# Optimization experiments

Hardware: AMD Instinct MI355X
Metric: run time of the kernel (lower is better)

The kernel has to match this reference:

```python
import jax, jax.numpy as jnp
import numpy as np
import math

B = 8
LATENT = 1024
K_DIM = 128   # conv input channels / view dim k
M_DIM = 256   # attention feature dim m
N = 4096      # points_num // num_branch; attention seq len
EPS = 1e-5


def _bn(h, g, b, m, v):
    # inference-mode BatchNorm1d over [B, C, L]
    return (h - m[None, :, None]) * (g / jnp.sqrt(v + EPS))[None, :, None] + b[None, :, None]


def _conv(h, w, b):
    # Conv1d with kernel_size=1 == channel matmul: h [B,C,L], w [O,C]
    return jnp.einsum('bcl,oc->bol', h, w) + b[None, :, None]


def setup_inputs() -> dict:
    key = jax.random.key(0)
    ks = jax.random.split(key, 64)
    it = iter(range(64))

    def nrm(shape, scale=0.05):
        return jax.random.normal(ks[next(it)], shape, jnp.float32) * scale

    def pos(shape):
        return jax.random.uniform(ks[next(it)], shape, jnp.float32, 0.5, 1.5)

    d = {}
    d['x'] = jax.random.normal(ks[next(it)], (B, LATENT), jnp.float32)
    d['fc1_w'] = nrm((M_DIM * K_DIM, LATENT))
    d['fc1_b'] = nrm((M_DIM * K_DIM,))
    d['c1q_w'] = nrm((64, K_DIM)); d['c1q_b'] = nrm((64,))
    d['c2q_w'] = nrm((128, 64));   d['c2q_b'] = nrm((128,))
    d['c3q_w'] = nrm((N, 128));    d['c3q_b'] = nrm((N,))
    d['c3k_w'] = nrm((N, 128));    d['c3k_b'] = nrm((N,))
    d['c1v_w'] = nrm((64, K_DIM)); d['c1v_b'] = nrm((64,))
    d['c2v_w'] = nrm((128, 64));   d['c2v_b'] = nrm((128,))
    d['c3v_w'] = nrm((N, 128));    d['c3v_b'] = nrm((N,))
    for nm, c in [('bn1q', 64), ('bn2q', 128), ('bn1k', 64), ('bn2k', 128), ('bn1v', 64), ('bn2v', 128)]:
        d[nm + '_g'] = pos((c,))
        d[nm + '_be'] = nrm((c,))
        d[nm + '_m'] = nrm((c,))
        d[nm + '_v'] = pos((c,))
    d['co_w'] = nrm((3, M_DIM)); d['co_b'] = nrm((3,))
    return d


def _forward(x, fc1_w, fc1_b, c1q_w, c1q_b, c2q_w, c2q_b, c3q_w, c3q_b, c3k_w, c3k_b,
             c1v_w, c1v_b, c2v_w, c2v_b, c3v_w, c3v_b,
             bn1q_g, bn1q_be, bn1q_m, bn1q_v, bn2q_g, bn2q_be, bn2q_m, bn2q_v,
             bn1k_g, bn1k_be, bn1k_m, bn1k_v, bn2k_g, bn2k_be, bn2k_m, bn2k_v,
             bn1v_g, bn1v_be, bn1v_m, bn1v_v, bn2v_g, bn2v_be, bn2v_m, bn2v_v,
             co_w, co_b):
    h = (x @ fc1_w.T + fc1_b).reshape(-1, M_DIM, K_DIM)   # [B, m, k]
    h = jnp.transpose(h, (0, 2, 1))                        # [B, k, m]
    # Q path
    Q = jax.nn.relu(_bn(_conv(h, c1q_w, c1q_b), bn1q_g, bn1q_be, bn1q_m, bn1q_v))
    Q = jax.nn.relu(_bn(_conv(Q, c2q_w, c2q_b), bn2q_g, bn2q_be, bn2q_m, bn2q_v))
    Q = _conv(Q, c3q_w, c3q_b)                             # [B, n, m]
    # K path: source re-uses conv1_q / conv2_q weights (faithful to original)
    K = jax.nn.relu(_bn(_conv(h, c1q_w, c1q_b), bn1k_g, bn1k_be, bn1k_m, bn1k_v))
    K = jax.nn.relu(_bn(_conv(K, c2q_w, c2q_b), bn2k_g, bn2k_be, bn2k_m, bn2k_v))
    K = _conv(K, c3k_w, c3k_b)                             # [B, n, m]
    # V path
    V = jax.nn.relu(_bn(_conv(h, c1v_w, c1v_b), bn1v_g, bn1v_be, bn1v_m, bn1v_v))
    V = jax.nn.relu(_bn(_conv(V, c2v_w, c2v_b), bn2v_g, bn2v_be, bn2v_m, bn2v_v))
    V = _conv(V, c3v_w, c3v_b)                             # [B, n, m]
    # hand-rolled attention: scores [B, n, n] (source scales by sqrt(k))
    scores = jnp.einsum('bim,bjm->bij', Q, K) / math.sqrt(K_DIM)
    attn = jax.nn.softmax(scores, axis=2)
    out = jnp.einsum('bij,bjm->bim', attn, V)              # [B, n, m]
    out = jnp.einsum('bnm,om->bon', out, co_w) + co_b[None, :, None]  # [B, 3, n]
    return jnp.transpose(out, (0, 2, 1))                   # [B, n, 3]


def reference(x, fc1_w, fc1_b, c1q_w, c1q_b, c2q_w, c2q_b, c3q_w, c3q_b, c3k_w, c3k_b,
              c1v_w, c1v_b, c2v_w, c2v_b, c3v_w, c3v_b,
              bn1q_g, bn1q_be, bn1q_m, bn1q_v, bn2q_g, bn2q_be, bn2q_m, bn2q_v,
              bn1k_g, bn1k_be, bn1k_m, bn1k_v, bn2k_g, bn2k_be, bn2k_m, bn2k_v,
              bn1v_g, bn1v_be, bn1v_m, bn1v_v, bn2v_g, bn2v_be, bn2v_m, bn2v_v,
              co_w, co_b):
    return _forward(x, fc1_w, fc1_b, c1q_w, c1q_b, c2q_w, c2q_b, c3q_w, c3q_b, c3k_w, c3k_b,
                    c1v_w, c1v_b, c2v_w, c2v_b, c3v_w, c3v_b,
                    bn1q_g, bn1q_be, bn1q_m, bn1q_v, bn2q_g, bn2q_be, bn2q_m, bn2q_v,
                    bn1k_g, bn1k_be, bn1k_m, bn1k_v, bn2k_g, bn2k_be, bn2k_m, bn2k_v,
                    bn1v_g, bn1v_be, bn1v_m, bn1v_v, bn2v_g, bn2v_be, bn2v_m, bn2v_v,
                    co_w, co_b)
```

## Files before the change

kernel.cpp:

```cpp
#include <hip/hip_runtime.h>
#include <cstdint>
#include <cstddef>

#define EPS 1e-5f

typedef __attribute__((ext_vector_type(8))) short bf16x8;
typedef __attribute__((ext_vector_type(4))) float f32x4;
typedef __attribute__((ext_vector_type(16))) float f32x16;

__device__ __forceinline__ unsigned short rne_bf16(float f) {
  union { float f; unsigned int u; } v; v.f = f;
  unsigned int u = v.u;
  return (unsigned short)((u + 0x7fffu + ((u >> 16) & 1u)) >> 16);
}
__device__ __forceinline__ float bf16_to_f(unsigned short h) {
  union { unsigned int u; float f; } v; v.u = ((unsigned int)h) << 16; return v.f;
}
__device__ __forceinline__ void split_hl(float v, unsigned short& h, unsigned short& l) {
  h = rne_bf16(v);
  l = rne_bf16(v - bf16_to_f(h));
}
__device__ __forceinline__ f32x4 mfma16(bf16x8 a, bf16x8 b, f32x4 c) {
  return __builtin_amdgcn_mfma_f32_16x16x32_bf16(a, b, c, 0, 0, 0);
}
__device__ __forceinline__ f32x16 mfma32(bf16x8 a, bf16x8 b, f32x16 c) {
  return __builtin_amdgcn_mfma_f32_32x32x16_bf16(a, b, c, 0, 0, 0);
}

__global__ __launch_bounds__(256) void k_fc1(const float* __restrict__ x,
                                             const float* __restrict__ w,
                                             const float* __restrict__ bias,
                                             float* __restrict__ h_t) {
  const int lane = threadIdx.x & 63;
  const int wv = threadIdx.x >> 6;
  const int r = blockIdx.x * 4 + wv;
  const float4* wr = (const float4*)(w + (size_t)r * 1024);
  float acc[8] = {0, 0, 0, 0, 0, 0, 0, 0};
#pragma unroll
  for (int i = 0; i < 4; ++i) {
    float4 wv4 = wr[lane + i * 64];
#pragma unroll
    for (int b = 0; b < 8; ++b) {
      float4 xv = ((const float4*)(x + b * 1024))[lane + i * 64];
      acc[b] += wv4.x * xv.x + wv4.y * xv.y + wv4.z * xv.z + wv4.w * xv.w;
    }
  }
#pragma unroll
  for (int d = 1; d < 64; d <<= 1) {
#pragma unroll
    for (int b = 0; b < 8; ++b) acc[b] += __shfl_xor(acc[b], d);
  }
  if (lane == 0) {
    const int mm = r >> 7, kk = r & 127;
    const float bb = bias[r];
#pragma unroll
    for (int b = 0; b < 8; ++b) h_t[b * 32768 + kk * 256 + mm] = acc[b] + bb;
  }
}

__global__ __launch_bounds__(256) void k_conv1(
    const float* __restrict__ h_t,
    const float* __restrict__ c1q_w, const float* __restrict__ c1q_b,
    const float* __restrict__ c1v_w, const float* __restrict__ c1v_b,
    const float* __restrict__ g1q, const float* __restrict__ be1q,
    const float* __restrict__ mu1q, const float* __restrict__ va1q,
    const float* __restrict__ g1k, const float* __restrict__ be1k,
    const float* __restrict__ mu1k, const float* __restrict__ va1k,
    const float* __restrict__ g1v, const float* __restrict__ be1v,
    const float* __restrict__ mu1v, const float* __restrict__ va1v,
    float* __restrict__ T1q, float* __restrict__ T1k, float* __restrict__ T1v) {
  const int m = threadIdx.x;
  const int o = blockIdx.x & 63;
  const int b = blockIdx.x >> 6;
  const int path = blockIdx.y;
  const float* w = (path == 0 ? c1q_w : c1v_w) + o * 128;
  const float* h = h_t + b * 32768 + m;
  float acc = 0.f;
#pragma unroll 8
  for (int c = 0; c < 128; ++c) acc += w[c] * h[c * 256];
  if (path == 0) {
    const float z = acc + c1q_b[o];
    const float sq = g1q[o] / sqrtf(va1q[o] + EPS);
    T1q[b * 16384 + o * 256 + m] = fmaxf((z - mu1q[o]) * sq + be1q[o], 0.f);
    const float sk = g1k[o] / sqrtf(va1k[o] + EPS);
    T1k[b * 16384 + o * 256 + m] = fmaxf((z - mu1k[o]) * sk + be1k[o], 0.f);
  } else {
    const float z = acc + c1v_b[o];
    const float sv = g1v[o] / sqrtf(va1v[o] + EPS);
    T1v[b * 16384 + o * 256 + m] = fmaxf((z - mu1v[o]) * sv + be1v[o], 0.f);
  }
}

__global__ __launch_bounds__(256) void k_conv2(
    const float* __restrict__ T1q, const float* __restrict__ T1k,
    const float* __restrict__ T1v,
    const float* __restrict__ c2q_w, const float* __restrict__ c2q_b,
    const float* __restrict__ c2v_w, const float* __restrict__ c2v_b,
    const float* __restrict__ g2q, const float* __restrict__ be2q,
    const float* __restrict__ mu2q, const float* __restrict__ va2q,
    const float* __restrict__ g2k, const float* __restrict__ be2k,
    const float* __restrict__ mu2k, const float* __restrict__ va2k,
    const float* __restrict__ g2v, const float* __restrict__ be2v,
    const float* __restrict__ mu2v, const float* __restrict__ va2v,
    unsigned short* __restrict__ Q2H, unsigned short* __restrict__ Q2L,
    unsigned short* __restrict__ K2H, unsigned short* __restrict__ K2L,
    float* __restrict__ V2F) {
  const int m = threadIdx.x;
  const int b = blockIdx.x;
  const int path = blockIdx.y;
  const int oc = blockIdx.z;
  const float* T1 = (path == 0 ? T1q : path == 1 ? T1k : T1v) + b * 16384 + m;
  const float* w = (path == 2 ? c2v_w : c2q_w);
  const float* cb = (path == 2 ? c2v_b : c2q_b);
  const float* g = (path == 0 ? g2q : path == 1 ? g2k : g2v);
  const float* be = (path == 0 ? be2q : path == 1 ? be2k : be2v);
  const float* mu = (path == 0 ? mu2q : path == 1 ? mu2k : mu2v);
  const float* va = (path == 0 ? va2q : path == 1 ? va2k : va2v);
  float t[64];
#pragma unroll
  for (int c = 0; c < 64; ++c) t[c] = T1[c * 256];
  unsigned short* oh =
      (path == 0 ? Q2H : K2H) + b * 32768 + m * 128 + oc * 64;
  unsigned short* ol =
      (path == 0 ? Q2L : K2L) + b * 32768 + m * 128 + oc * 64;
  for (int og = 0; og < 8; ++og) {
    bf16x8 ph, pl;
#pragma unroll
    for (int j = 0; j < 8; ++j) {
      const int o = oc * 64 + og * 8 + j;
      float acc = cb[o];
      const float* wo = w + o * 64;
#pragma unroll
      for (int c = 0; c < 64; ++c) acc += wo[c] * t[c];
      const float s = g[o] / sqrtf(va[o] + EPS);
      const float val = fmaxf((acc - mu[o]) * s + be[o], 0.f);
      if (path == 2) {
        V2F[b * 32768 + o * 256 + m] = val;
      } else {
        unsigned short hh, ll;
        split_hl(val, hh, ll);
        ph[j] = (short)hh; pl[j] = (short)ll;
      }
    }
    if (path != 2) {
      *(bf16x8*)(oh + og * 8) = ph;
      *(bf16x8*)(ol + og * 8) = pl;
    }
  }
}

__global__ __launch_bounds__(256) void k_conv3all(
    const float* __restrict__ c3q_w, const float* __restrict__ c3q_b,
    const float* __restrict__ c3k_w, const float* __restrict__ c3k_b,
    const unsigned short* __restrict__ Q2H, const unsigned short* __restrict__ Q2L,
    const unsigned short* __restrict__ K2H, const unsigned short* __restrict__ K2L,
    unsigned short* __restrict__ QhB, unsigned short* __restrict__ QlB,
    unsigned short* __restrict__ KhB, unsigned short* __restrict__ KlB,
    const float* __restrict__ c3v_w, const float* __restrict__ c3v_b,
    const float* __restrict__ V2F, const float* __restrict__ co_w,
    float4* __restrict__ Vpp) {
  const int z = blockIdx.z;
  const int b = blockIdx.y;
  if (z == 2) {
    if (blockIdx.x >= 16) return;
    __shared__ float Us[387];
    __shared__ float Up[256][3];
    const int tt = threadIdx.x;
    {
      const int c = tt >> 1, mh = tt & 1;
      const float* v = V2F + b * 32768 + c * 256 + mh * 128;
      const float* cw0 = co_w + mh * 128;
      float u0 = 0.f, u1 = 0.f, u2 = 0.f;
#pragma unroll 4
      for (int mm = 0; mm < 128; ++mm) {
        const float xv = v[mm];
        u0 += xv * cw0[mm];
        u1 += xv * cw0[256 + mm];
        u2 += xv * cw0[512 + mm];
      }
      Up[tt][0] = u0; Up[tt][1] = u1; Up[tt][2] = u2;
      if (tt < 3) {
        float s = 0.f;
        for (int mm = 0; mm < 256; ++mm) s += co_w[tt * 256 + mm];
        Us[384 + tt] = s;
      }
    }
    __syncthreads();
    if ((tt & 1) == 0) {
      const int c = tt >> 1;
      Us[c * 3 + 0] = Up[tt][0] + Up[tt + 1][0];
      Us[c * 3 + 1] = Up[tt][1] + Up[tt + 1][1];
      Us[c * 3 + 2] = Up[tt][2] + Up[tt + 1][2];
    }
    __syncthreads();
    const int n = blockIdx.x * 256 + tt;
    const float* w = c3v_w + (size_t)n * 128;
    float a0 = 0.f, a1 = 0.f, a2 = 0.f;
#pragma unroll 4
    for (int c = 0; c < 128; ++c) {
      const float wc = w[c];
      a0 += wc * Us[c * 3 + 0];
      a1 += wc * Us[c * 3 + 1];
      a2 += wc * Us[c * 3 + 2];
    }
    const float bb = c3v_b[n];
    Vpp[(size_t)b * 4096 + n] =
        make_float4(a0 + bb * Us[384], a1 + bb * Us[385], a2 + bb * Us[386], 0.f);
    return;
  }
  const float* W = (z == 0) ? c3q_w : c3k_w;
  const float* bias = (z == 0) ? c3q_b : c3k_b;
  const unsigned short* Xh = (z == 0) ? Q2H : K2H;
  const unsigned short* Xl = (z == 0) ? Q2L : K2L;
  unsigned short* Yh = (z == 0) ? QhB : KhB;
  unsigned short* Yl = (z == 0) ? QlB : KlB;
  const float scale = (z == 0) ? 0.08838834764831845f * 1.4426950408889634f : 1.0f;
  const int lane = threadIdx.x & 63, wv = threadIdx.x >> 6;
  const int l15 = lane & 15, quad = lane >> 4;
  const unsigned short* XH = Xh + b * 32768;
  const unsigned short* XL = Xl + b * 32768;
  unsigned short* YH = Yh + (size_t)b * 4096 * 256;
  unsigned short* YL = Yl + (size_t)b * 4096 * 256;
  const int nb = blockIdx.x * 64 + wv * 16;
  const float* wr = W + (size_t)(nb + l15) * 128 + quad * 8;
  bf16x8 ah[4], al[4];
#pragma unroll
  for (int ks = 0; ks < 4; ++ks) {
#pragma unroll
    for (int j = 0; j < 8; ++j) {
      unsigned short hh, ll;
      split_hl(wr[ks * 32 + j], hh, ll);
      ah[ks][j] = (short)hh; al[ks][j] = (short)ll;
    }
  }
  f32x4 acc[16];
#pragma unroll
  for (int ms = 0; ms < 16; ++ms) acc[ms] = (f32x4){0, 0, 0, 0};
#pragma unroll
  for (int ks = 0; ks < 4; ++ks) {
#pragma unroll
    for (int ms = 0; ms < 16; ++ms) {
      const size_t off = (size_t)(ms * 16 + l15) * 128 + ks * 32 + quad * 8;
      bf16x8 bh = *(const bf16x8*)(XH + off);
      bf16x8 bl = *(const bf16x8*)(XL + off);
      acc[ms] = mfma16(ah[ks], bh, acc[ms]);
      acc[ms] = mfma16(al[ks], bh, acc[ms]);
      acc[ms] = mfma16(ah[ks], bl, acc[ms]);
    }
  }
#pragma unroll
  for (int r = 0; r < 4; ++r) {
    const int n = nb + quad * 4 + r;
    const float bv = bias[n];
#pragma unroll
    for (int ms = 0; ms < 16; ++ms) {
      const float v = (acc[ms][r] + bv) * scale;
      unsigned short hh, ll;
      split_hl(v, hh, ll);
      YH[(size_t)n * 256 + ms * 16 + l15] = hh;
      YL[(size_t)n * 256 + ms * 16 + l15] = ll;
    }
  }
}

__global__ __launch_bounds__(256, 2) void k_attn(
    const unsigned short* __restrict__ Qh, const unsigned short* __restrict__ Ql,
    const unsigned short* __restrict__ Kh, const unsigned short* __restrict__ Kl,
    const float4* __restrict__ Vpp, float4* __restrict__ part) {
  __shared__ __align__(16) short Kt[2][2][32 * 264];
  __shared__ __align__(16) float4 Vt[2][32];
  const int t = threadIdx.x;
  const int lane = t & 63, wv = t >> 6;
  const int l31 = lane & 31, half = lane >> 5;
  const int b = blockIdx.x & 7;
  const int qt = (blockIdx.x >> 3) & 31;
  const int jh = blockIdx.x >> 8;
  const int qrow = qt * 128 + wv * 32 + l31;
  const size_t qoff = ((size_t)b * 4096 + qrow) * 256 + half * 8;
  bf16x8 qfh[16], qfl[16];
#pragma unroll
  for (int kc = 0; kc < 16; ++kc) {
    qfh[kc] = *(const bf16x8*)(Qh + qoff + kc * 16);
    qfl[kc] = *(const bf16x8*)(Ql + qoff + kc * 16);
  }
  const unsigned short* Kgh = Kh + (size_t)b * 4096 * 256;
  const unsigned short* Kgl = Kl + (size_t)b * 4096 * 256;
  const float4* Vg = Vpp + (size_t)b * 4096;
  const int r0 = t >> 5;
  const int sseg = (t & 31) * 8;
  float a0 = 0.f, a1 = 0.f, a2 = 0.f, al = 0.f;
  const int jt0 = jh * 64;
  {
    const int jbase = jt0 * 32;
#pragma unroll
    for (int i = 0; i < 4; ++i) {
      const int row = i * 8 + r0;
      const size_t g = (size_t)(jbase + row) * 256 + sseg;
      *(bf16x8*)&Kt[0][0][row * 264 + sseg] = *(const bf16x8*)(Kgh + g);
      *(bf16x8*)&Kt[0][1][row * 264 + sseg] = *(const bf16x8*)(Kgl + g);
    }
    if (t < 32) Vt[0][t] = Vg[jbase + t];
  }
  __syncthreads();
  for (int it = 0; it < 64; ++it) {
    const int cur = it & 1, nxt = cur ^ 1;
    const bool pf = (it < 63);
    bf16x8 th[4], tl[4];
    float4 vpf = make_float4(0.f, 0.f, 0.f, 0.f);
    if (pf) {
      const int jb2 = (jt0 + it + 1) * 32;
#pragma unroll
      for (int i = 0; i < 4; ++i) {
        const size_t g = (size_t)(jb2 + i * 8 + r0) * 256 + sseg;
        th[i] = *(const bf16x8*)(Kgh + g);
        tl[i] = *(const bf16x8*)(Kgl + g);
      }
      if (t < 32) vpf = Vg[jb2 + t];
    }
    f32x16 sA, sB;
#pragma unroll
    for (int r = 0; r < 16; ++r) { sA[r] = 0.f; sB[r] = 0.f; }
    const short* KH = Kt[cur][0];
    const short* KL = Kt[cur][1];
#pragma unroll
    for (int kc = 0; kc < 16; ++kc) {
      bf16x8 kh = *(const bf16x8*)&KH[l31 * 264 + kc * 16 + half * 8];
      bf16x8 kl = *(const bf16x8*)&KL[l31 * 264 + kc * 16 + half * 8];
      sA = mfma32(kh, qfh[kc], sA);
      sB = mfma32(kh, qfl[kc], sB);
      sA = mfma32(kl, qfh[kc], sA);
    }
#pragma unroll
    for (int r = 0; r < 16; ++r) {
      const float p = __builtin_amdgcn_exp2f(sA[r] + sB[r]);
      const float4 vj = Vt[cur][(r & 3) + 8 * (r >> 2) + 4 * half];
      a0 += p * vj.x; a1 += p * vj.y; a2 += p * vj.z; al += p;
    }
    if (pf) {
#pragma unroll
      for (int i = 0; i < 4; ++i) {
        const int row = i * 8 + r0;
        *(bf16x8*)&Kt[nxt][0][row * 264 + sseg] = th[i];
        *(bf16x8*)&Kt[nxt][1][row * 264 + sseg] = tl[i];
      }
      if (t < 32) Vt[nxt][t] = vpf;
    }
    __syncthreads();
  }
  a0 += __shfl_xor(a0, 32);
  a1 += __shfl_xor(a1, 32);
  a2 += __shfl_xor(a2, 32);
  al += __shfl_xor(al, 32);
  if (half == 0)
    part[(size_t)jh * 32768 + (size_t)b * 4096 + qrow] =
        make_float4(a0, a1, a2, al);
}

__global__ __launch_bounds__(256) void k_combine(
    const float4* __restrict__ part, const float* __restrict__ co_b,
    float* __restrict__ out) {
  const int i = blockIdx.x * 256 + threadIdx.x;
  const float4 pa = part[i];
  const float4 pb = part[32768 + i];
  const float rl = 1.f / (pa.w + pb.w);
  const float b0 = co_b[0], b1 = co_b[1], b2 = co_b[2];
  out[(size_t)i * 3 + 0] = (pa.x + pb.x) * rl + b0;
  out[(size_t)i * 3 + 1] = (pa.y + pb.y) * rl + b1;
  out[(size_t)i * 3 + 2] = (pa.z + pb.z) * rl + b2;
}

extern "C" void kernel_launch(void* const* d_in, const int* in_sizes, int n_in,
                              void* d_out, int out_size, void* d_ws, size_t ws_size,
                              hipStream_t stream) {
  const float* x = (const float*)d_in[0];
  const float* fc1_w = (const float*)d_in[1];
  const float* fc1_b = (const float*)d_in[2];
  const float* c1q_w = (const float*)d_in[3];
  const float* c1q_b = (const float*)d_in[4];
  const float* c2q_w = (const float*)d_in[5];
  const float* c2q_b = (const float*)d_in[6];
  const float* c3q_w = (const float*)d_in[7];
  const float* c3q_b = (const float*)d_in[8];
  const float* c3k_w = (const float*)d_in[9];
  const float* c3k_b = (const float*)d_in[10];
  const float* c1v_w = (const float*)d_in[11];
  const float* c1v_b = (const float*)d_in[12];
  const float* c2v_w = (const float*)d_in[13];
  const float* c2v_b = (const float*)d_in[14];
  const float* c3v_w = (const float*)d_in[15];
  const float* c3v_b = (const float*)d_in[16];
  const float* bn1q_g = (const float*)d_in[17];
  const float* bn1q_be = (const float*)d_in[18];
  const float* bn1q_m = (const float*)d_in[19];
  const float* bn1q_v = (const float*)d_in[20];
  const float* bn2q_g = (const float*)d_in[21];
  const float* bn2q_be = (const float*)d_in[22];
  const float* bn2q_m = (const float*)d_in[23];
  const float* bn2q_v = (const float*)d_in[24];
  const float* bn1k_g = (const float*)d_in[25];
  const float* bn1k_be = (const float*)d_in[26];
  const float* bn1k_m = (const float*)d_in[27];
  const float* bn1k_v = (const float*)d_in[28];
  const float* bn2k_g = (const float*)d_in[29];
  const float* bn2k_be = (const float*)d_in[30];
  const float* bn2k_m = (const float*)d_in[31];
  const float* bn2k_v = (const float*)d_in[32];
  const float* bn1v_g = (const float*)d_in[33];
  const float* bn1v_be = (const float*)d_in[34];
  const float* bn1v_m = (const float*)d_in[35];
  const float* bn1v_v = (const float*)d_in[36];
  const float* bn2v_g = (const float*)d_in[37];
  const float* bn2v_be = (const float*)d_in[38];
  const float* bn2v_m = (const float*)d_in[39];
  const float* bn2v_v = (const float*)d_in[40];
  const float* co_w = (const float*)d_in[41];
  const float* co_b = (const float*)d_in[42];

  char* ws = (char*)d_ws;
  float* h_t = (float*)(ws + 0);
  float* T1q = (float*)(ws + 1048576);
  float* T1k = (float*)(ws + 1572864);
  float* T1v = (float*)(ws + 2097152);
  unsigned short* Q2H = (unsigned short*)(ws + 2621440);
  unsigned short* Q2L = (unsigned short*)(ws + 3145728);
  unsigned short* K2H = (unsigned short*)(ws + 3670016);
  unsigned short* K2L = (unsigned short*)(ws + 4194304);
  float* V2F = (float*)(ws + 4718592);
  unsigned short* QhB = (unsigned short*)(ws + 5767168);
  unsigned short* QlB = (unsigned short*)(ws + 22544384);
  unsigned short* KhB = (unsigned short*)(ws + 39321600);
  unsigned short* KlB = (unsigned short*)(ws + 56098816);
  float4* Vpp = (float4*)(ws + 72876032);
  float4* part = (float4*)(ws + 73416704);

  k_fc1<<<8192, 256, 0, stream>>>(x, fc1_w, fc1_b, h_t);
  k_conv1<<<dim3(512, 2), 256, 0, stream>>>(
      h_t, c1q_w, c1q_b, c1v_w, c1v_b,
      bn1q_g, bn1q_be, bn1q_m, bn1q_v,
      bn1k_g, bn1k_be, bn1k_m, bn1k_v,
      bn1v_g, bn1v_be, bn1v_m, bn1v_v,
      T1q, T1k, T1v);
  k_conv2<<<dim3(8, 3, 2), 256, 0, stream>>>(
      T1q, T1k, T1v, c2q_w, c2q_b, c2v_w, c2v_b,
      bn2q_g, bn2q_be, bn2q_m, bn2q_v,
      bn2k_g, bn2k_be, bn2k_m, bn2k_v,
      bn2v_g, bn2v_be, bn2v_m, bn2v_v,
      Q2H, Q2L, K2H, K2L, V2F);
  k_conv3all<<<dim3(64, 8, 3), 256, 0, stream>>>(
      c3q_w, c3q_b, c3k_w, c3k_b, Q2H, Q2L, K2H, K2L,
      QhB, QlB, KhB, KlB, c3v_w, c3v_b, V2F, co_w, Vpp);
  k_attn<<<512, 256, 0, stream>>>(QhB, QlB, KhB, KlB, Vpp, part);
  k_combine<<<128, 256, 0, stream>>>(part, co_b, (float*)d_out);
}
```

Measured before the change: 666.8 us.

## Fuse split-K combine into attention via atomics and add independent MFMA accumulator

Removes the separate combine kernel. Each of the two key-range blocks now atomically adds its partial numerator and denominator into a zeroed buffer, and the second block to finish, found through an atomic counter, normalises and writes the output. A third accumulator breaks the dependent MFMA chain on sA, and s_setprio raises wave priority around the MFMA loop. In exchange it adds a memset launch, atomic traffic and an extra register tile, which may pressure occupancy.

```diff
diff --git a/kernel.cpp b/kernel.cpp
--- a/kernel.cpp
+++ b/kernel.cpp
@@ -266,7 +266,9 @@
 __global__ __launch_bounds__(256, 2) void k_attn(
     const unsigned short* __restrict__ Qh, const unsigned short* __restrict__ Ql,
     const unsigned short* __restrict__ Kh, const unsigned short* __restrict__ Kl,
-    const float4* __restrict__ Vpp, float4* __restrict__ part) {
+    const float4* __restrict__ Vpp, float* __restrict__ partsum,
+    unsigned int* __restrict__ cnt, const float* __restrict__ co_b,
+    float* __restrict__ out) {
   __shared__ __align__(16) short Kt[2][2][32 * 264];
   __shared__ __align__(16) float4 Vt[2][32];
   const int t = threadIdx.x;
@@ -317,22 +319,24 @@
       }
       if (t < 32) vpf = Vg[jb2 + t];
     }
-    f32x16 sA, sB;
-#pragma unroll
-    for (int r = 0; r < 16; ++r) { sA[r] = 0.f; sB[r] = 0.f; }
+    f32x16 sA, sB, sC;
+#pragma unroll
+    for (int r = 0; r < 16; ++r) { sA[r] = 0.f; sB[r] = 0.f; sC[r] = 0.f; }
     const short* KH = Kt[cur][0];
     const short* KL = Kt[cur][1];
+    __builtin_amdgcn_s_setprio(1);
 #pragma unroll
     for (int kc = 0; kc < 16; ++kc) {
       bf16x8 kh = *(const bf16x8*)&KH[l31 * 264 + kc * 16 + half * 8];
       bf16x8 kl = *(const bf16x8*)&KL[l31 * 264 + kc * 16 + half * 8];
       sA = mfma32(kh, qfh[kc], sA);
       sB = mfma32(kh, qfl[kc], sB);
-      sA = mfma32(kl, qfh[kc], sA);
-    }
+      sC = mfma32(kl, qfh[kc], sC);
+    }
+    __builtin_amdgcn_s_setprio(0);
 #pragma unroll
     for (int r = 0; r < 16; ++r) {
-      const float p = __builtin_amdgcn_exp2f(sA[r] + sB[r]);
+      const float p = __builtin_amdgcn_exp2f(sA[r] + sB[r] + sC[r]);
       const float4 vj = Vt[cur][(r & 3) + 8 * (r >> 2) + 4 * half];
       a0 += p * vj.x; a1 += p * vj.y; a2 += p * vj.z; al += p;
     }
@@ -351,22 +355,26 @@
   a1 += __shfl_xor(a1, 32);
   a2 += __shfl_xor(a2, 32);
   al += __shfl_xor(al, 32);
-  if (half == 0)
-    part[(size_t)jh * 32768 + (size_t)b * 4096 + qrow] =
-        make_float4(a0, a1, a2, al);
-}
-
-__global__ __launch_bounds__(256) void k_combine(
-    const float4* __restrict__ part, const float* __restrict__ co_b,
-    float* __restrict__ out) {
-  const int i = blockIdx.x * 256 + threadIdx.x;
-  const float4 pa = part[i];
-  const float4 pb = part[32768 + i];
-  const float rl = 1.f / (pa.w + pb.w);
-  const float b0 = co_b[0], b1 = co_b[1], b2 = co_b[2];
-  out[(size_t)i * 3 + 0] = (pa.x + pb.x) * rl + b0;
-  out[(size_t)i * 3 + 1] = (pa.y + pb.y) * rl + b1;
-  out[(size_t)i * 3 + 2] = (pa.z + pb.z) * rl + b2;
+  if (half == 0) {
+    const int idx = b * 4096 + qrow;
+    float* ps = partsum + (size_t)idx * 4;
+    atomicAdd(ps + 0, a0);
+    atomicAdd(ps + 1, a1);
+    atomicAdd(ps + 2, a2);
+    atomicAdd(ps + 3, al);
+    __threadfence();
+    const unsigned int old = atomicAdd(&cnt[idx], 1u);
+    if (old == 1u) {
+      const float s0 = atomicAdd(ps + 0, 0.f);
+      const float s1 = atomicAdd(ps + 1, 0.f);
+      const float s2 = atomicAdd(ps + 2, 0.f);
+      const float sl = atomicAdd(ps + 3, 0.f);
+      const float rl = 1.f / sl;
+      out[(size_t)idx * 3 + 0] = s0 * rl + co_b[0];
+      out[(size_t)idx * 3 + 1] = s1 * rl + co_b[1];
+      out[(size_t)idx * 3 + 2] = s2 * rl + co_b[2];
+    }
+  }
 }
 
 extern "C" void kernel_launch(void* const* d_in, const int* in_sizes, int n_in,
@@ -431,7 +439,10 @@
   unsigned short* KhB = (unsigned short*)(ws + 39321600);
   unsigned short* KlB = (unsigned short*)(ws + 56098816);
   float4* Vpp = (float4*)(ws + 72876032);
-  float4* part = (float4*)(ws + 73416704);
+  float* partsum = (float*)(ws + 73416704);
+  unsigned int* cnt = (unsigned int*)(ws + 73940992);
+
+  hipMemsetAsync(ws + 73416704, 0, 524288 + 131072, stream);
 
   k_fc1<<<8192, 256, 0, stream>>>(x, fc1_w, fc1_b, h_t);
   k_conv1<<<dim3(512, 2), 256, 0, stream>>>(
@@ -449,6 +460,6 @@
   k_conv3all<<<dim3(64, 8, 3), 256, 0, stream>>>(
       c3q_w, c3q_b, c3k_w, c3k_b, Q2H, Q2L, K2H, K2L,
       QhB, QlB, KhB, KlB, c3v_w, c3v_b, V2F, co_w, Vpp);
-  k_attn<<<512, 256, 0, stream>>>(QhB, QlB, KhB, KlB, Vpp, part);
-  k_combine<<<128, 256, 0, stream>>>(part, co_b, (float*)d_out);
-}
+  k_attn<<<512, 256, 0, stream>>>(QhB, QlB, KhB, KlB, Vpp, partsum, cnt,
+                                  co_b, (float*)d_out);
+}
```

After: 707.0 us. 6.0% more time.
